# Optimization experiments

Measured on AMD Instinct MI355X. Metric: run time of the kernel, lower is better.

## Reference

```python
import jax, jax.numpy as jnp
import numpy as np

N, C, H, T, D, K = 4096, 512, 128, 64, 20, 10


def setup_inputs() -> dict:
    key = jax.random.key(0)
    ks = jax.random.split(key, 40)
    s = 0.05
    inp = {}
    inp["x"] = jax.random.normal(ks[0], (N, D * T), jnp.float32)
    inp["concept_matrix"] = (jax.random.uniform(ks[1], (N, C)) < 0.05).astype(jnp.float32)
    inp["market_value"] = jax.random.uniform(ks[2], (N,), jnp.float32) + 0.1
    # GRU params (torch layout: w_ih [3H,in], w_hh [3H,H], biases [3H]); 2 layers
    inp["gru_w_ih0"] = jax.random.normal(ks[3], (3 * H, D), jnp.float32) * s
    inp["gru_w_hh0"] = jax.random.normal(ks[4], (3 * H, H), jnp.float32) * s
    inp["gru_b_ih0"] = jax.random.normal(ks[5], (3 * H,), jnp.float32) * s
    inp["gru_b_hh0"] = jax.random.normal(ks[6], (3 * H,), jnp.float32) * s
    inp["gru_w_ih1"] = jax.random.normal(ks[7], (3 * H, H), jnp.float32) * s
    inp["gru_w_hh1"] = jax.random.normal(ks[8], (3 * H, H), jnp.float32) * s
    inp["gru_b_ih1"] = jax.random.normal(ks[9], (3 * H,), jnp.float32) * s
    inp["gru_b_hh1"] = jax.random.normal(ks[10], (3 * H,), jnp.float32) * s
    names = ["ps", "hs", "ps_fore", "hs_fore", "ps_back", "hs_back", "indi"]
    for i, n in enumerate(names):
        inp["w_" + n] = jax.random.normal(ks[11 + 2 * i], (H, H), jnp.float32) * s
        inp["b_" + n] = jax.random.normal(ks[12 + 2 * i], (H,), jnp.float32) * s
    inp["w_out"] = jax.random.normal(ks[30], (1, H), jnp.float32) * s
    inp["b_out"] = jax.random.normal(ks[31], (1,), jnp.float32) * s
    return inp


def _cos_sim(x, y):
    # x [n,d], y [m,d] -> [n,m]; NaN (0/0) replaced by 0 via safe denominator
    xy = x @ y.T
    nx = jnp.sqrt(jnp.sum(x * x, axis=1))[:, None]
    ny = jnp.sqrt(jnp.sum(y * y, axis=1))[:, None]
    return xy / jnp.maximum(nx @ ny.T, 1e-12)


def _gru_layer(seq, wih, whh, bih, bhh):
    # seq [T, n, in] -> outputs [T, n, H]
    n = seq.shape[1]
    h0 = jnp.zeros((n, whh.shape[1]), seq.dtype)

    def step(h, xt):
        gx = xt @ wih.T + bih
        gh = h @ whh.T + bhh
        gxr, gxz, gxn = jnp.split(gx, 3, axis=1)
        ghr, ghz, ghn = jnp.split(gh, 3, axis=1)
        r = jax.nn.sigmoid(gxr + ghr)
        z = jax.nn.sigmoid(gxz + ghz)
        ncand = jnp.tanh(gxn + r * ghn)
        hnew = (1.0 - z) * ncand + z * h
        return hnew, hnew

    _, out = jax.lax.scan(step, h0, seq)
    return out


def reference(x, concept_matrix, market_value,
              gru_w_ih0, gru_w_hh0, gru_b_ih0, gru_b_hh0,
              gru_w_ih1, gru_w_hh1, gru_b_ih1, gru_b_hh1,
              w_ps, b_ps, w_hs, b_hs, w_ps_fore, b_ps_fore, w_hs_fore, b_hs_fore,
              w_ps_back, b_ps_back, w_hs_back, b_hs_back, w_indi, b_indi,
              w_out, b_out):
    n = x.shape[0]
    # [n, D*T] -> [n, D, T] -> [n, T, D] -> [T, n, D]
    seq = jnp.swapaxes(x.reshape(n, D, -1).transpose(0, 2, 1), 0, 1)
    out0 = _gru_layer(seq, gru_w_ih0, gru_w_hh0, gru_b_ih0, gru_b_hh0)
    out1 = _gru_layer(out0, gru_w_ih1, gru_w_hh1, gru_b_ih1, gru_b_hh1)
    x_hidden = out1[-1]  # [n, H]

    # --- predefined-concept branch ---
    s2c = concept_matrix * market_value[:, None]
    s2c_den = jnp.sum(s2c, axis=0)[None, :] * concept_matrix + 1.0
    s2c = s2c / s2c_den
    hidden = s2c.T @ x_hidden  # [C, H]
    v1 = jnp.sum(hidden, axis=1) != 0  # valid concepts (replaces row filtering)
    s2c2 = jax.nn.softmax(x_hidden @ hidden.T, axis=0)  # [n, C], column-wise
    hidden2 = s2c2.T @ x_hidden  # [C, H]
    c2s = _cos_sim(x_hidden, hidden2)
    c2s = jax.nn.softmax(jnp.where(v1[None, :], c2s, -1e9), axis=1) * v1[None, :]
    p_shared = c2s @ hidden2
    p_shared = p_shared @ w_ps.T + b_ps
    p_back = p_shared @ w_ps_back.T + b_ps_back
    out_ps = jax.nn.leaky_relu(p_shared @ w_ps_fore.T + b_ps_fore)

    # --- hidden-concept branch ---
    h_shared = x_hidden - p_back
    hs2c = _cos_sim(h_shared, h_shared)  # [n, n]
    diag = jnp.diagonal(hs2c)
    hs2c = hs2c * (1.0 - jnp.eye(n, dtype=hs2c.dtype))
    _, idx = jax.lax.top_k(hs2c, K)  # [n, K]
    mask = jnp.zeros_like(hs2c).at[jnp.arange(n)[:, None], idx].set(1.0)
    hs2c = hs2c * mask
    hs2c = hs2c + jnp.diag((jnp.sum(hs2c, axis=0) != 0).astype(hs2c.dtype) * diag)
    hidden_h = (h_shared.T @ hs2c).T  # [n, H]
    v2 = jnp.sum(hidden_h, axis=1) != 0
    hc2s = _cos_sim(h_shared, hidden_h)
    hc2s = jax.nn.softmax(jnp.where(v2[None, :], hc2s, -1e9), axis=1) * v2[None, :]
    h_si = hc2s @ hidden_h
    h_si = h_si @ w_hs.T + b_hs
    h_back = h_si @ w_hs_back.T + b_hs_back
    out_hs = jax.nn.leaky_relu(h_si @ w_hs_fore.T + b_hs_fore)

    # --- individual branch + head ---
    indi = x_hidden - p_back - h_back
    out_indi = jax.nn.leaky_relu(indi @ w_indi.T + b_indi)
    all_info = out_ps + out_hs + out_indi
    return (all_info @ w_out.T + b_out).squeeze()
```

## Files before the change

### kernel.cpp

```cpp
#include <hip/hip_runtime.h>
#include <cstddef>

#define NR 4096
#define CDIM 512
#define HDIM 128
#define TSTEPS 64
#define DDIM 20
#define KTOP 10

typedef __attribute__((ext_vector_type(8))) short short8;
typedef __attribute__((ext_vector_type(4))) float f32x4;

__device__ __forceinline__ unsigned short f2bf(float f) {
    union { float f; unsigned u; } x; x.f = f;
    unsigned r = (x.u + 0x7fffu + ((x.u >> 16) & 1u)) >> 16;
    return (unsigned short)r;
}
__device__ __forceinline__ unsigned short f2bf_t(float f) {
    union { float f; unsigned u; } x; x.f = f;
    return (unsigned short)(x.u >> 16);
}
__device__ __forceinline__ float bf2f(unsigned short h) {
    union { unsigned u; float f; } x; x.u = ((unsigned)h) << 16;
    return x.f;
// ... 158 lines not shown
        #pragma unroll
        for (int j = 0; j < 8; j++) {
            float f = src[(size_t)(kb + j) * HDIM + n];
            unsigned short h = f2bf(f);
            knh[(size_t)idx * 8 + j] = h;
            knl[(size_t)idx * 8 + j] = f2bf_t(f - bf2f(h));
        }
    }
}

struct PAll {
    const float* wb_src[4];
    unsigned short* wb_dst[4];
    const float* w7_src[7];
    unsigned short* w7_hi[7];
    unsigned short* w7_lo[7];
};
__global__ void pack_all(PAll p)
{
    int idx = blockIdx.x * 256 + threadIdx.x;
    const int WB_END = 1536 + 3 * 6144;
    if (idx < WB_END) {
        int m, base, nch, K;
        if (idx < 1536) { m = 0; base = 0; nch = 1; K = DDIM; }
        else {
            int q = (idx - 1536) / 6144;
            m = 1 + q;
            base = 1536 + q * 6144;
            nch = 4; K = HDIM;
        }
        int r = idx - base;
        int lane = r & 63;
        int c = (r >> 6) % nch;
        int t = r / (nch * 64);
        int n = t * 16 + (lane & 15);
        int kb = c * 32 + (lane >> 4) * 8;
        const float* W = p.wb_src[m];
        unsigned short* Wp = p.wb_dst[m];
        #pragma unroll
        for (int j = 0; j < 8; j++) {
            int k = kb + j;
            float f = (k < K) ? W[(size_t)n * K + k] : 0.f;
            Wp[(size_t)r * 8 + j] = f2bf(f);
        }
    } else {
        int q = idx - WB_END;
        if (q >= 7 * 2048) return;
        int m = q >> 11;
        int r = q & 2047;
        int lane = r & 63;
        int c = (r >> 6) & 3;
        int t = r >> 8;
        int n = (t << 4) + (lane & 15);
        int kb = (c << 5) + ((lane >> 4) << 3);
        const float* src = p.w7_src[m];
        unsigned short* hi = p.w7_hi[m];
        unsigned short* lo = p.w7_lo[m];
        #pragma unroll
        for (int j = 0; j < 8; j++) {
            float f = src[(size_t)n * HDIM + kb + j];
            unsigned short h = f2bf(f);
            hi[(size_t)r * 8 + j] = h;
            lo[(size_t)r * 8 + j] = f2bf_t(f - bf2f(h));
        }
    }
}

__global__ __launch_bounds__(256) void scan_topk(const float* __restrict__ S,
        const float* __restrict__ hn, float* __restrict__ diagv,
        float* __restrict__ tvals, int* __restrict__ tidx)
{
    int row = blockIdx.x;
    const float* d = S + (size_t)row * NR;
    int tid = threadIdx.x;
    int wv = tid >> 6, lane = tid & 63;
    float hi_ = hn[row];
    float lv[16];
    #pragma unroll
    for (int i = 0; i < 16; i++) {
        int j = tid + (i << 8);
        float v = d[j] / fmaxf(hi_ * hn[j], 1e-12f);
        if (j == row) { diagv[row] = v; v = 0.f; }
        lv[i] = v;
    }
    __shared__ float sv[4];
    __shared__ int si[4];
    for (int k = 0; k < KTOP; k++) {
        float bv = -INFINITY; int bi = 0x7fffffff;
        #pragma unroll
        for (int i = 0; i < 16; i++) {
            int j = tid + (i << 8);
            if (lv[i] > bv || (lv[i] == bv && j < bi)) { bv = lv[i]; bi = j; }
        }
        #pragma unroll
        for (int m = 1; m < 64; m <<= 1) {
            float ov = __shfl_xor(bv, m); int oi = __shfl_xor(bi, m);
            if (ov > bv || (ov == bv && oi < bi)) { bv = ov; bi = oi; }
        }
        if (lane == 0) { sv[wv] = bv; si[wv] = bi; }
        __syncthreads();
        bv = sv[0]; bi = si[0];
        #pragma unroll
        for (int w = 1; w < 4; w++) {
            float ov = sv[w]; int oi = si[w];
            if (ov > bv || (ov == bv && oi < bi)) { bv = ov; bi = oi; }
        }
        if (tid == 0) { tvals[row * KTOP + k] = bv; tidx[row * KTOP + k] = bi; }
        if ((bi & 255) == tid) lv[bi >> 8] = -INFINITY;
        __syncthreads();
    }
}

__global__ __launch_bounds__(512) void hc2s_flash(
    const float* __restrict__ hsh, const float* __restrict__ hn,
    const float* __restrict__ hhn, const float* __restrict__ v2,
    const unsigned short* __restrict__ Bh, const unsigned short* __restrict__ Bl,
    const unsigned short* __restrict__ Vh, const unsigned short* __restrict__ Vl,
    float* __restrict__ pO, float* __restrict__ pM, float* __restrict__ pL)
{
    __shared__ __attribute__((aligned(16))) unsigned short Ph[8][16 * 72];
    __shared__ __attribute__((aligned(16))) unsigned short Plo[8][16 * 72];

    const int tid = threadIdx.x;
    const int wv = tid >> 6, lane = tid & 63, quad = lane >> 4, lm = lane & 15;
    const int rg2 = wv >> 1;
    const int cc = wv & 1;
    const int bm = (blockIdx.x << 6) + (rg2 << 4);
    const int rgg = (blockIdx.x << 2) + rg2;
    const int pidx = (blockIdx.y << 1) + cc;
    const int jt0 = (blockIdx.y << 4) + (cc << 3);

    short8 ahh[4], ahl[4];
    #pragma unroll
    for (int c = 0; c < 4; c++) {
        const float* ap = hsh + (size_t)(bm + lm) * HDIM + (c << 5) + (quad << 3);
        float4 a0 = *(const float4*)ap;
        float4 a1 = *(const float4*)(ap + 4);
        #pragma unroll
        for (int j = 0; j < 4; j++) {
            float f = (&a0.x)[j];
            unsigned short h = f2bf(f);
            ahh[c][j] = h; ahl[c][j] = f2bf_t(f - bf2f(h));
            f = (&a1.x)[j];
            h = f2bf(f);
            ahh[c][4 + j] = h; ahl[c][4 + j] = f2bf_t(f - bf2f(h));
        }
    }
    float hnr[4];
    #pragma unroll
    for (int rg = 0; rg < 4; rg++) hnr[rg] = hn[bm + (quad << 2) + rg];

    float m_old[4], l_old[4];
    #pragma unroll
    for (int rg = 0; rg < 4; rg++) { m_old[rg] = -INFINITY; l_old[rg] = 0.f; }
    f32x4 o[8];
    #pragma unroll
    for (int vt = 0; vt < 8; vt++) o[vt] = (f32x4){0.f, 0.f, 0.f, 0.f};

    const int pwr = lm * 72;
    for (int it = 0; it < 8; it++) {
        const int jt = jt0 + it;
        f32x4 s[4];
        #pragma unroll
        for (int tg = 0; tg < 4; tg++) {
            s[tg] = (f32x4){0.f, 0.f, 0.f, 0.f};
            #pragma unroll
            for (int c = 0; c < 4; c++) {
                size_t bidx = ((size_t)(((jt << 2) + tg) * 4 + c) * 64 + lane) * 8;
                short8 bh = *(const short8*)(Bh + bidx);
                short8 bl = *(const short8*)(Bl + bidx);
                s[tg] = MFMA16(ahh[c], bh, s[tg]);
                s[tg] = MFMA16(ahh[c], bl, s[tg]);
                s[tg] = MFMA16(ahl[c], bh, s[tg]);
            }
        }
        float sv[4][4];
        #pragma unroll
        for (int tg = 0; tg < 4; tg++) {
            int col = (jt << 6) + (tg << 4) + lm;
            float hc = hhn[col];
            float vm = v2[col];
            #pragma unroll
            for (int rg = 0; rg < 4; rg++) {
                float v = s[tg][rg] * __builtin_amdgcn_rcpf(fmaxf(hnr[rg] * hc, 1e-12f));
                sv[tg][rg] = (vm == 0.f) ? -1e9f : v;
            }
        }
        float m_new[4], alpha[4], tsum[4], pv[4][4];
        #pragma unroll
        for (int rg = 0; rg < 4; rg++) {
            float m = fmaxf(fmaxf(sv[0][rg], sv[1][rg]), fmaxf(sv[2][rg], sv[3][rg]));
            #pragma unroll
            for (int d = 1; d < 16; d <<= 1) m = fmaxf(m, __shfl_xor(m, d));
            m_new[rg] = fmaxf(m_old[rg], m);
            alpha[rg] = __expf(m_old[rg] - m_new[rg]);
        }
        #pragma unroll
        for (int rg = 0; rg < 4; rg++) {
            float p0_ = __expf(sv[0][rg] - m_new[rg]);
            float p1_ = __expf(sv[1][rg] - m_new[rg]);
            float p2_ = __expf(sv[2][rg] - m_new[rg]);
            float p3_ = __expf(sv[3][rg] - m_new[rg]);
            pv[0][rg] = p0_; pv[1][rg] = p1_; pv[2][rg] = p2_; pv[3][rg] = p3_;
            float ss = p0_ + p1_ + p2_ + p3_;
            #pragma unroll
            for (int d = 1; d < 16; d <<= 1) ss += __shfl_xor(ss, d);
            tsum[rg] = ss;
        }
        #pragma unroll
        for (int rg = 0; rg < 4; rg++) {
            l_old[rg] = l_old[rg] * alpha[rg] + tsum[rg];
            m_old[rg] = m_new[rg];
        }
        #pragma unroll
        for (int vt = 0; vt < 8; vt++) {
            #pragma unroll
            for (int rg = 0; rg < 4; rg++) o[vt][rg] *= alpha[rg];
        }
        #pragma unroll
        for (int tg = 0; tg < 4; tg++) {
            #pragma unroll
            for (int rg = 0; rg < 4; rg++) {
                int off = ((quad << 2) + rg) * 72 + (tg << 4) + lm;
                float p = pv[tg][rg];
                unsigned short h = f2bf(p);
                Ph[wv][off] = h;
                Plo[wv][off] = f2bf_t(p - bf2f(h));
            }
        }
        __asm__ volatile("s_waitcnt lgkmcnt(0)" ::: "memory");
        #pragma unroll
        for (int c2 = 0; c2 < 2; c2++) {
            int poff = pwr + (c2 << 5) + (quad << 3);
            short8 pah = *(const short8*)&Ph[wv][poff];
            short8 pal = *(const short8*)&Plo[wv][poff];
            int cg = (jt << 1) + c2;
            #pragma unroll
            for (int vt = 0; vt < 8; vt++) {
                size_t b0 = ((size_t)(vt * 128 + cg) * 64 + lane) * 8;
                short8 vh = *(const short8*)(Vh + b0);
                short8 vl = *(const short8*)(Vl + b0);
                o[vt] = MFMA16(pah, vh, o[vt]);
                o[vt] = MFMA16(pah, vl, o[vt]);
                o[vt] = MFMA16(pal, vh, o[vt]);
            }
        }
    }
    size_t pb = ((size_t)rgg * 8 + pidx) * 16;
    #pragma unroll
    for (int rg = 0; rg < 4; rg++) {
        int r = (quad << 2) + rg;
        #pragma unroll
        for (int vt = 0; vt < 8; vt++)
            pO[(pb + r) * 128 + (vt << 4) + lm] = o[vt][rg];
    }
    if (lm == 0) {
        #pragma unroll
        for (int rg = 0; rg < 4; rg++) {
            int r = (quad << 2) + rg;
            pM[pb + r] = m_old[rg];
            pL[pb + r] = l_old[rg];
        }
    }
}

__global__ __launch_bounds__(256) void hc2s_merge(const float* __restrict__ pO,
        const float* __restrict__ pM, const float* __restrict__ pL,
        float* __restrict__ O)
{
    int rgg = blockIdx.x;
    int tid = threadIdx.x;
    int r = tid >> 4;
    int c0 = (tid & 15) << 3;
    float m[8], e[8];
    float M = -INFINITY;
    #pragma unroll
    for (int i = 0; i < 8; i++) {
        m[i] = pM[((size_t)rgg * 8 + i) * 16 + r];
        M = fmaxf(M, m[i]);
    }
    float L = 0.f;
    #pragma unroll
    for (int i = 0; i < 8; i++) {
        e[i] = __expf(m[i] - M);
        L += pL[((size_t)rgg * 8 + i) * 16 + r] * e[i];
    }
    float invL = __builtin_amdgcn_rcpf(L);
    float a[8];
    #pragma unroll
    for (int k = 0; k < 8; k++) a[k] = 0.f;
    #pragma unroll
    for (int i = 0; i < 8; i++) {
        const float* src = pO + (((size_t)rgg * 8 + i) * 16 + r) * 128 + c0;
        float4 v0 = *(const float4*)src;
        float4 v1 = *(const float4*)(src + 4);
        a[0] += v0.x * e[i]; a[1] += v0.y * e[i]; a[2] += v0.z * e[i]; a[3] += v0.w * e[i];
        a[4] += v1.x * e[i]; a[5] += v1.y * e[i]; a[6] += v1.z * e[i]; a[7] += v1.w * e[i];
    }
    float* dst = O + ((size_t)rgg * 16 + r) * 128 + c0;
    #pragma unroll
    for (int k = 0; k < 8; k++) dst[k] = a[k] * invL;
}

__global__ __launch_bounds__(512, 2) void gru_mfma(
    const float* __restrict__ xg,
    const unsigned short* __restrict__ wih0p,
    const unsigned short* __restrict__ whh0p,
    const unsigned short* __restrict__ wih1p,
    const unsigned short* __restrict__ whh1p,
    const float* __restrict__ bih0, const float* __restrict__ bhh0,
    const float* __restrict__ bih1, const float* __restrict__ bhh1,
    float* __restrict__ xh)
{
    __shared__ __attribute__((aligned(16))) unsigned short h0A[2][2][16 * 136];
    __shared__ __attribute__((aligned(16))) unsigned short h1A[2][2][16 * 136];
    __shared__ __attribute__((aligned(16))) unsigned short xA[2][2][16 * 40];

    const int tid = threadIdx.x;
    const int w2 = tid >> 6;
    const int lane = tid & 63;
    const int quad = lane >> 4;
    const int lm = lane & 15;
    const int n0 = blockIdx.x << 4;
    const int j = (w2 << 4) + lm;

    for (int i = tid; i < 2 * 2 * 16 * 136; i += 512) {
        ((unsigned short*)h0A)[i] = 0;
        ((unsigned short*)h1A)[i] = 0;
    }
    for (int i = tid; i < 2 * 2 * 16 * 40; i += 512) ((unsigned short*)xA)[i] = 0;

    float br0 = bih0[j] + bhh0[j];
    float bz0 = bih0[128 + j] + bhh0[128 + j];
    float bni0 = bih0[256 + j];
    float bnh0 = bhh0[256 + j];
    float br1 = bih1[j] + bhh1[j];
    float bz1 = bih1[128 + j] + bhh1[128 + j];
    float bni1 = bih1[256 + j];
    float bnh1 = bhh1[256 + j];

    short8 W0x[3], W0h[3][4], W1x[3][4], W1h[3][4];
    {
        const int lb = lane * 8;
        W0x[0] = *(const short8*)&wih0p[(size_t)(w2) * 512 + lb];
        W0x[1] = *(const short8*)&wih0p[(size_t)(8 + w2) * 512 + lb];
        W0x[2] = *(const short8*)&wih0p[(size_t)(16 + w2) * 512 + lb];
        #pragma unroll
        for (int c = 0; c < 4; c++) {
            W0h[0][c] = *(const short8*)&whh0p[(size_t)((w2) * 4 + c) * 512 + lb];
            W0h[1][c] = *(const short8*)&whh0p[(size_t)((8 + w2) * 4 + c) * 512 + lb];
            W0h[2][c] = *(const short8*)&whh0p[(size_t)((16 + w2) * 4 + c) * 512 + lb];
            W1x[0][c] = *(const short8*)&wih1p[(size_t)((w2) * 4 + c) * 512 + lb];
            W1x[1][c] = *(const short8*)&wih1p[(size_t)((8 + w2) * 4 + c) * 512 + lb];
            W1x[2][c] = *(const short8*)&wih1p[(size_t)((16 + w2) * 4 + c) * 512 + lb];
            W1h[0][c] = *(const short8*)&whh1p[(size_t)((w2) * 4 + c) * 512 + lb];
            W1h[1][c] = *(const short8*)&whh1p[(size_t)((8 + w2) * 4 + c) * 512 + lb];
            W1h[2][c] = *(const short8*)&whh1p[(size_t)((16 + w2) * 4 + c) * 512 + lb];
        }
    }

    const int aoff = lm * 136 + quad * 8;
    const int xoff = lm * 40 + quad * 8;
    const bool stager = tid < 16 * DDIM;
    const int sn = tid / DDIM, sd = tid % DDIM;
    const float* xrow = xg + (size_t)(n0 + sn) * (DDIM * TSTEPS) + sd * TSTEPS;
    const int soff = sn * 40 + sd;

    float h0reg[4] = {0.f, 0.f, 0.f, 0.f};
    float h1reg[4] = {0.f, 0.f, 0.f, 0.f};

    if (stager) {
        float v0 = xrow[0], v1 = xrow[1];
        unsigned short a = f2bf_t(v0);
        xA[0][0][soff] = a; xA[0][1][soff] = f2bf_t(v0 - bf2f(a));
        unsigned short b = f2bf_t(v1);
        xA[1][0][soff] = b; xA[1][1][soff] = f2bf_t(v1 - bf2f(b));
    }
    __syncthreads();

    {
        f32x4 accr = (f32x4){br0, br0, br0, br0};
        f32x4 accz = (f32x4){bz0, bz0, bz0, bz0};
        f32x4 accni = (f32x4){bni0, bni0, bni0, bni0};
        short8 axh = *(const short8*)&xA[0][0][xoff];
        short8 axl = *(const short8*)&xA[0][1][xoff];
        accr = MFMA16(axh, W0x[0], accr);
        accz = MFMA16(axh, W0x[1], accz);
        accni = MFMA16(axh, W0x[2], accni);
        accr = MFMA16(axl, W0x[0], accr);
        accz = MFMA16(axl, W0x[1], accz);
        accni = MFMA16(axl, W0x[2], accni);
        #pragma unroll
        for (int rg = 0; rg < 4; rg++) {
            float r = sigm(accr[rg]);
            float z = sigm(accz[rg]);
            float nc = tanh_f(accni[rg] + r * bnh0);
            float hnew = nc - z * nc;
            h0reg[rg] = hnew;
            int off = (quad * 4 + rg) * 136 + j;
            unsigned short hh_ = f2bf_t(hnew);
            h0A[0][0][off] = hh_;
            h0A[0][1][off] = f2bf_t(hnew - bf2f(hh_));
        }
    }
    __syncthreads();

#define GRU_IT(B, DO_L0, XT, LAST)                                                \
{                                                                                 \
    float xv = 0.f;                                                               \
    if ((XT) >= 0 && stager) xv = xrow[XT];          \
    f32x4 accr0 = (f32x4){br0, br0, br0, br0};                                    \
    f32x4 accz0 = (f32x4){bz0, bz0, bz0, bz0};                                    \
    f32x4 accni0 = (f32x4){bni0, bni0, bni0, bni0};                               \
    f32x4 accnh0 = (f32x4){bnh0, bnh0, bnh0, bnh0};                               \
    f32x4 accr1 = (f32x4){br1, br1, br1, br1};                                    \
    f32x4 accz1 = (f32x4){bz1, bz1, bz1, bz1};                                    \
    f32x4 accni1 = (f32x4){bni1, bni1, bni1, bni1};                               \
    f32x4 accnh1 = (f32x4){bnh1, bnh1, bnh1, bnh1};                               \
    if (DO_L0) {                                                                  \
        short8 axh = *(const short8*)&xA[(B) ^ 1][0][xoff];                       \
        short8 axl = *(const short8*)&xA[(B) ^ 1][1][xoff];                       \
        accr0 = MFMA16(axh, W0x[0], accr0);                                       \
        accz0 = MFMA16(axh, W0x[1], accz0);                                       \
        accni0 = MFMA16(axh, W0x[2], accni0);                                     \
        accr0 = MFMA16(axl, W0x[0], accr0);                                       \
        accz0 = MFMA16(axl, W0x[1], accz0);                                       \
        accni0 = MFMA16(axl, W0x[2], accni0);                                     \
    }                                                                             \
    _Pragma("unroll")                                                             \
    for (int c = 0; c < 4; c++) {                                                 \
        short8 a0h = *(const short8*)&h0A[B][0][aoff + c * 32];                   \
        short8 a0l = *(const short8*)&h0A[B][1][aoff + c * 32];                   \
        short8 a1h = *(const short8*)&h1A[(B) ^ 1][0][aoff + c * 32];             \
        short8 a1l = *(const short8*)&h1A[(B) ^ 1][1][aoff + c * 32];             \
                \
        if (DO_L0) {                                                              \
            accr0 = MFMA16(a0h, W0h[0][c], accr0);                                \
            accz0 = MFMA16(a0h, W0h[1][c], accz0);                                \
            accnh0 = MFMA16(a0h, W0h[2][c], accnh0);                              \
        }                                                                         \
        accr1 = MFMA16(a0h, W1x[0][c], accr1);                                    \
        accz1 = MFMA16(a0h, W1x[1][c], accz1);                                    \
        accni1 = MFMA16(a0h, W1x[2][c], accni1);                                  \
                                                                    \
        if (DO_L0) {                                                              \
            accr0 = MFMA16(a0l, W0h[0][c], accr0);                                \
            accz0 = MFMA16(a0l, W0h[1][c], accz0);                                \
            accnh0 = MFMA16(a0l, W0h[2][c], accnh0);                              \
        }                                                                         \
        accr1 = MFMA16(a0l, W1x[0][c], accr1);                                    \
        accz1 = MFMA16(a0l, W1x[1][c], accz1);                                    \
        accni1 = MFMA16(a0l, W1x[2][c], accni1);                                  \
                                                                    \
        accr1 = MFMA16(a1h, W1h[0][c], accr1);                                    \
        accz1 = MFMA16(a1h, W1h[1][c], accz1);                                    \
        accnh1 = MFMA16(a1h, W1h[2][c], accnh1);                                  \
                                                                    \
        accr1 = MFMA16(a1l, W1h[0][c], accr1);                                    \
        accz1 = MFMA16(a1l, W1h[1][c], accz1);                                    \
        accnh1 = MFMA16(a1l, W1h[2][c], accnh1);                                  \
    }                                                                             \
    if (DO_L0) {                                                                  \
        _Pragma("unroll")                                                         \
        for (int rg = 0; rg < 4; rg++) {                                          \
            float r = sigm(accr0[rg]);                                            \
            float z = sigm(accz0[rg]);                                            \
            float nc = tanh_f(accni0[rg] + r * accnh0[rg]);                       \
            float hnew = nc + z * (h0reg[rg] - nc);                               \
            h0reg[rg] = hnew;                                                     \
            int off = (quad * 4 + rg) * 136 + j;                                  \
            unsigned short hh_ = f2bf_t(hnew);                                    \
            h0A[(B) ^ 1][0][off] = hh_;                                           \
            h0A[(B) ^ 1][1][off] = f2bf_t(hnew - bf2f(hh_));                      \
        }                                                                         \
    }                                                                             \
    _Pragma("unroll")                                                             \
    for (int rg = 0; rg < 4; rg++) {                                              \
        float r = sigm(accr1[rg]);                                                \
        float z = sigm(accz1[rg]);                                                \
        float nc = tanh_f(accni1[rg] + r * accnh1[rg]);                           \
        float hnew = nc + z * (h1reg[rg] - nc);                                   \
        h1reg[rg] = hnew;                                                         \
        if (LAST) {                                                               \
            xh[(size_t)(n0 + quad * 4 + rg) * HDIM + j] = hnew;                   \
        } else {                                                                  \
            int off = (quad * 4 + rg) * 136 + j;                                  \
            unsigned short hh_ = f2bf_t(hnew);                                    \
            h1A[B][0][off] = hh_;                                                 \
            h1A[B][1][off] = f2bf_t(hnew - bf2f(hh_));                            \
        }                                                                         \
    }                                                                             \
    if ((XT) >= 0 && stager) {                                                    \
        unsigned short hh_ = f2bf_t(xv);                                          \
        xA[B][0][soff] = hh_;                                                     \
        xA[B][1][soff] = f2bf_t(xv - bf2f(hh_));                                  \
    }                                                                             \
    if (!(LAST)) __syncthreads();                                                 \
}

    for (int i = 0; i < 62; i += 2) {
        GRU_IT(0, true, i + 2, false)
        GRU_IT(1, true, i + 3, false)
    }
    GRU_IT(0, true, -1, false)
    GRU_IT(1, false, -1, true)
#undef GRU_IT
}

__global__ __launch_bounds__(256) void den_atomic(const float* __restrict__ cm,
        const float* __restrict__ mv, float* __restrict__ den)
{
    int c = blockIdx.x * 64 + (threadIdx.x & 63);
    int rg = threadIdx.x >> 6;
    int nbase = blockIdx.y * 128;
    float acc = 0.f;
    for (int i = 0; i < 32; i++) {
        int n = nbase + rg + (i << 2);
        acc += cm[(size_t)n * CDIM + c] * mv[n];
    }
    __shared__ float red[4][64];
    red[rg][threadIdx.x & 63] = acc;
    __syncthreads();
    if (rg == 0)
        atomicAdd(&den[c], red[0][threadIdx.x] + red[1][threadIdx.x] +
                           red[2][threadIdx.x] + red[3][threadIdx.x]);
}

__global__ __launch_bounds__(256) void s2ct_trans(const float* __restrict__ cm,
        const float* __restrict__ mv, const float* __restrict__ den,
        float* __restrict__ s2cT)
{
    __shared__ float tile[64][65];
    __shared__ float mvs[64];
    const int tid = threadIdx.x;
    const int n0 = blockIdx.x << 6;
    const int c0 = blockIdx.y << 6;
    const int lc = tid & 63, lr = tid >> 6;
    if (tid < 64) mvs[tid] = mv[n0 + tid];
    #pragma unroll
    for (int i = 0; i < 16; i++) {
        int n = lr + (i << 2);
        tile[n][lc] = cm[(size_t)(n0 + n) * CDIM + c0 + lc];
    }
    __syncthreads();
    #pragma unroll
    for (int i = 0; i < 16; i++) {
        int c = lr + (i << 2);
        float m = tile[lc][c];
        float d = den[c0 + c];
        s2cT[(size_t)(c0 + c) * NR + n0 + lc] = (m * mvs[lc]) / (d * m + 1.f);
    }
}

__global__ void row_norm(const float* __restrict__ a, float* __restrict__ out)
{
    int r = blockIdx.x;
    float acc = 0.f;
    for (int h = threadIdx.x; h < HDIM; h += 64) {
        float v = a[(size_t)r * HDIM + h];
        acc += v * v;
    }
    for (int o = 32; o > 0; o >>= 1) acc += __shfl_down(acc, o);
    if (threadIdx.x == 0) out[r] = sqrtf(acc);
}

__global__ void row_nonzero(const float* __restrict__ a, float* __restrict__ out)
{
    int r = blockIdx.x;
    float acc = 0.f;
    for (int h = threadIdx.x; h < HDIM; h += 64) acc += a[(size_t)r * HDIM + h];
    for (int o = 32; o > 0; o >>= 1) acc += __shfl_down(acc, o);
    if (threadIdx.x == 0) out[r] = (acc != 0.f) ? 1.f : 0.f;
}

__global__ void row_norm_nz(const float* __restrict__ a, float* __restrict__ nrm,
                            float* __restrict__ nz)
{
    int r = blockIdx.x;
    float acc = 0.f, s = 0.f;
    for (int h = threadIdx.x; h < HDIM; h += 64) {
        float v = a[(size_t)r * HDIM + h];
        acc += v * v;
        s += v;
    }
    for (int o = 32; o > 0; o >>= 1) { acc += __shfl_down(acc, o); s += __shfl_down(s, o); }
    if (threadIdx.x == 0) { nrm[r] = sqrtf(acc); nz[r] = (s != 0.f) ? 1.f : 0.f; }
}

__global__ __launch_bounds__(256) void cos_softmax_row(float* __restrict__ data, int N,
        const float* __restrict__ rn, const float* __restrict__ cn,
        const float* __restrict__ vmask)
{
    int row = blockIdx.x;
    float* d = data + (size_t)row * N;
    int tid = threadIdx.x;
    int wv = tid >> 6, lane = tid & 63;
    __shared__ float red[8];
    float rnv = rn ? rn[row] : 0.f;
    float mx = -INFINITY;
    for (int j = tid; j < N; j += 256) {
        float v = d[j];
        if (cn) v = v * __builtin_amdgcn_rcpf(fmaxf(rnv * cn[j], 1e-12f));
        if (vmask && vmask[j] == 0.f) v = -1e9f;
        d[j] = v;
        mx = fmaxf(mx, v);
    }
    #pragma unroll
    for (int m = 1; m < 64; m <<= 1) mx = fmaxf(mx, __shfl_xor(mx, m));
    if (lane == 0) red[wv] = mx;
    __syncthreads();
    float M = fmaxf(fmaxf(red[0], red[1]), fmaxf(red[2], red[3]));
    float sum = 0.f;
    for (int j = tid; j < N; j += 256) {
        float e = __expf(d[j] - M);
        d[j] = e;
        sum += e;
    }
    #pragma unroll
    for (int m = 1; m < 64; m <<= 1) sum += __shfl_xor(sum, m);
    if (lane == 0) red[4 + wv] = sum;
    __syncthreads();
    float inv = __builtin_amdgcn_rcpf(red[4] + red[5] + red[6] + red[7]);
    for (int j = tid; j < N; j += 256) {
        float v = d[j] * inv;
        if (vmask) v *= vmask[j];
        d[j] = v;
    }
}

__global__ void hh_scatter(const float* __restrict__ vals, const int* __restrict__ idxs,
                           const float* __restrict__ hsh, float* __restrict__ hh,
                           float* __restrict__ colsum)
{
    int i = blockIdx.x;
    int t = threadIdx.x;
    float hv = hsh[(size_t)i * HDIM + t];
    #pragma unroll
    for (int k = 0; k < KTOP; k++) {
        int p = i * KTOP + k;
        int jj = idxs[p];
        float v = vals[p];
        atomicAdd(&hh[(size_t)jj * HDIM + t], v * hv);
    }
    if (t < KTOP) {
        int p = i * KTOP + t;
        atomicAdd(&colsum[idxs[p]], vals[p]);
    }
}

__global__ void hh_diag(const float* __restrict__ colsum, const float* __restrict__ diag,
                        const float* __restrict__ hsh, float* __restrict__ hh)
{
    int idx = blockIdx.x * 256 + threadIdx.x;
    int j = idx >> 7;
    if (colsum[j] != 0.f) hh[idx] += diag[j] * hsh[idx];
}

static inline void mg(hipStream_t s, const float* A, const unsigned short* Bh,
                      const unsigned short* Bl, const float* bias, float* C,
                      int M, int N, int K, int z, int flags,
                      const float* aux = nullptr, float* sub = nullptr,
                      const unsigned short* Ah = nullptr, const unsigned short* Al = nullptr,
                      const float* wout = nullptr, const float* bout = nullptr,
                      float* hout = nullptr)
{
    MG g{A, Bh, Bl, bias, C, aux, sub, Ah, Al,
         nullptr, nullptr, nullptr, nullptr, wout, bout, hout,
         N, K, K / z, flags | (z > 1 ? 4 : 0) | (Ah ? 16 : 0), 0};
    mfma_gemm<<<dim3(N / 64, M / 64, z), 256, 0, s>>>(g);
}
static inline void mg_dual(hipStream_t s, const float* A,
                           const unsigned short* Bh, const unsigned short* Bl,
                           const float* bias, float* C, int flags1,
                           const unsigned short* Bh2, const unsigned short* Bl2,
                           const float* bias2, float* C2, int flags2,
                           int M, int N, int K,
                           const float* aux, float* sub,
                           const float* wout, const float* bout, float* hout)
{
    MG g{A, Bh, Bl, bias, C, aux, sub, nullptr, nullptr,
         Bh2, Bl2, bias2, C2, wout, bout, hout,
         N, K, K, flags1 | 32, flags2};
    mfma_gemm<<<dim3(N / 64, M / 64, 2), 256, 0, s>>>(g);
}
static inline void pbt(hipStream_t s, const float* src, unsigned short* hi,
                       unsigned short* lo, int N, int K)
{
    int total = (N / 16) * (K / 32) * 64;
    pack_bt<<<(total + 255) / 256, 256, 0, s>>>(src, hi, lo, K, total);
}
static inline void pboth(hipStream_t s, const float* src,
                         unsigned short* bth, unsigned short* btl,
                         unsigned short* knh, unsigned short* knl, int N)
{
    int totBT = (N / 16) * 4 * 64;
    int totKN = 8 * (N / 32) * 64;
    int tot = totBT > totKN ? totBT : totKN;
    pack_both<<<(tot + 255) / 256, 256, 0, s>>>(src, bth, btl, knh, knl, N, totKN);
}

extern "C" void kernel_launch(void* const* d_in, const int* in_sizes, int n_in,
                              void* d_out, int out_size, void* d_ws, size_t ws_size,
                              hipStream_t stream)
{
    (void)in_sizes; (void)n_in; (void)out_size; (void)ws_size;
    const float* x    = (const float*)d_in[0];
    const float* cm   = (const float*)d_in[1];
    const float* mv   = (const float*)d_in[2];
    const float* wih0 = (const float*)d_in[3];
    const float* whh0 = (const float*)d_in[4];
    const float* bih0 = (const float*)d_in[5];
    const float* bhh0 = (const float*)d_in[6];
    const float* wih1 = (const float*)d_in[7];
    const float* whh1 = (const float*)d_in[8];
    const float* bih1 = (const float*)d_in[9];
    const float* bhh1 = (const float*)d_in[10];
    const float* w_ps = (const float*)d_in[11];
    const float* b_ps = (const float*)d_in[12];
    const float* w_hs = (const float*)d_in[13];
    const float* b_hs = (const float*)d_in[14];
    const float* w_ps_fore = (const float*)d_in[15];
    const float* b_ps_fore = (const float*)d_in[16];
    const float* w_hs_fore = (const float*)d_in[17];
    const float* b_hs_fore = (const float*)d_in[18];
    const float* w_ps_back = (const float*)d_in[19];
    const float* b_ps_back = (const float*)d_in[20];
    const float* w_hs_back = (const float*)d_in[21];
    const float* b_hs_back = (const float*)d_in[22];
    const float* w_indi = (const float*)d_in[23];
    const float* b_indi = (const float*)d_in[24];
    const float* w_out  = (const float*)d_in[25];
    const float* b_out  = (const float*)d_in[26];
    float* out = (float*)d_out;

    float* ws = (float*)d_ws;
    float* BIG = ws;
    float* zero0 = ws + 16777216;
    float* den      = zero0;
    float* hidden   = den + 512;
    float* hidden2  = hidden + 65536;
    float* colsum   = hidden2 + 65536;
    float* p0       = colsum + 4096;
    float* hidden_h = p0 + 524288;
    float* p_shared = hidden_h + 524288;
    float* h_si     = p_shared + 524288;
    const size_t ZERO_FLOATS = 512 + 65536 + 65536 + 4096 + 4 * 524288;
    float* h1 = h_si + 524288;
    float* v1 = h1 + 524288;
    float* xnorm = v1 + 512;
    float* h2n = xnorm + 4096;
    float* p_back = h2n + 512;
    float* h_shared = p_back + 524288;
    float* hn = h_shared + 524288;
    float* diagv = hn + 4096;
    float* tvals = diagv + 4096;
    int*   tidx = (int*)(tvals + 40960);
    float* v2 = (float*)(tidx + 40960);
    float* hhn = v2 + 4096;
    float* hsi0 = hhn + 4096;
    float* h_back = hsi0 + 524288;
    float* indi = h_back + 524288;
    float* extra = indi + 524288;

    unsigned short* wih0p = (unsigned short*)(BIG + 5242880);
    unsigned short* whh0p = wih0p + 12288;
    unsigned short* wih1p = whh0p + 49152;
    unsigned short* whh1p = wih1p + 49152;
    float* s2cT = BIG;
    float* L    = BIG + 2097152;
    float* c2s  = BIG + 4194304;
    unsigned short* PB = (unsigned short*)(BIG + 6291456);
    unsigned short* pbt_xh_hi = PB;
    unsigned short* pbt_xh_lo = pbt_xh_hi + 524288;
    unsigned short* pkn_xh_hi = pbt_xh_lo + 524288;
    unsigned short* pkn_xh_lo = pkn_xh_hi + 524288;
    unsigned short* pbt_h2_hi = pkn_xh_lo + 524288;
    unsigned short* pbt_h2_lo = pbt_h2_hi + 65536;
    unsigned short* pkn_h2_hi = pbt_h2_lo + 65536;
    unsigned short* pkn_h2_lo = pkn_h2_hi + 65536;
    unsigned short* wps_hi  = pkn_h2_lo + 65536;
    unsigned short* wps_lo  = wps_hi + 16384;
    unsigned short* wpsb_hi = wps_lo + 16384;
    unsigned short* wpsb_lo = wpsb_hi + 16384;
    unsigned short* wpsf_hi = wpsb_lo + 16384;
    unsigned short* wpsf_lo = wpsf_hi + 16384;
    unsigned short* pbt_hsh_hi = (unsigned short*)p0;
    unsigned short* pbt_hsh_lo = pbt_hsh_hi + 524288;
    unsigned short* pbt_hh_hi = (unsigned short*)indi;
    unsigned short* pbt_hh_lo = pbt_hh_hi + 524288;
    unsigned short* pkn_hh_hi = (unsigned short*)hsi0;
    unsigned short* pkn_hh_lo = pkn_hh_hi + 524288;
    float* part_O = BIG;
    float* part_m = BIG + 4194304;
    float* part_l = BIG + 4227072;
    unsigned short* EX = (unsigned short*)extra;
    unsigned short* whs_hi  = EX;            unsigned short* whs_lo  = EX + 16384;
    unsigned short* whsb_hi = EX + 32768;    unsigned short* whsb_lo = EX + 49152;
    unsigned short* whsf_hi = EX + 65536;    unsigned short* whsf_lo = EX + 81920;
    unsigned short* wind_hi = EX + 98304;    unsigned short* wind_lo = EX + 114688;

    hipMemsetAsync(zero0, 0, ZERO_FLOATS * sizeof(float), stream);
    hipMemsetAsync(out, 0, NR * sizeof(float), stream);

    {
        PAll pa;
        pa.wb_src[0] = wih0; pa.wb_dst[0] = wih0p;
        pa.wb_src[1] = whh0; pa.wb_dst[1] = whh0p;
        pa.wb_src[2] = wih1; pa.wb_dst[2] = wih1p;
        pa.wb_src[3] = whh1; pa.wb_dst[3] = whh1p;
        pa.w7_src[0] = w_ps;      pa.w7_hi[0] = wps_hi;  pa.w7_lo[0] = wps_lo;
        pa.w7_src[1] = w_ps_back; pa.w7_hi[1] = wpsb_hi; pa.w7_lo[1] = wpsb_lo;
        pa.w7_src[2] = w_ps_fore; pa.w7_hi[2] = wpsf_hi; pa.w7_lo[2] = wpsf_lo;
        pa.w7_src[3] = w_hs;      pa.w7_hi[3] = whs_hi;  pa.w7_lo[3] = whs_lo;
        pa.w7_src[4] = w_hs_back; pa.w7_hi[4] = whsb_hi; pa.w7_lo[4] = whsb_lo;
        pa.w7_src[5] = w_hs_fore; pa.w7_hi[5] = whsf_hi; pa.w7_lo[5] = whsf_lo;
        pa.w7_src[6] = w_indi;    pa.w7_hi[6] = wind_hi; pa.w7_lo[6] = wind_lo;
        pack_all<<<134, 256, 0, stream>>>(pa);
    }
    gru_mfma<<<NR / 16, 512, 0, stream>>>(x, wih0p, whh0p, wih1p, whh1p,
                                          bih0, bhh0, bih1, bhh1, h1);
    float* x_hidden = h1;

    den_atomic<<<dim3(CDIM / 64, 32), 256, 0, stream>>>(cm, mv, den);
    s2ct_trans<<<dim3(NR / 64, CDIM / 64), 256, 0, stream>>>(cm, mv, den, s2cT);
    pboth(stream, x_hidden, pbt_xh_hi, pbt_xh_lo, pkn_xh_hi, pkn_xh_lo, NR);
    mg(stream, s2cT, pkn_xh_hi, pkn_xh_lo, nullptr, hidden, CDIM, HDIM, NR, 16, 0);
    row_nonzero<<<CDIM, 64, 0, stream>>>(hidden, v1);
    mg(stream, hidden, pbt_xh_hi, pbt_xh_lo, nullptr, L, CDIM, NR, HDIM, 1, 0);
    cos_softmax_row<<<CDIM, 256, 0, stream>>>(L, NR, nullptr, nullptr, nullptr);
    mg(stream, L, pkn_xh_hi, pkn_xh_lo, nullptr, hidden2, CDIM, HDIM, NR, 16, 0);
    row_norm<<<NR, 64, 0, stream>>>(x_hidden, xnorm);
    row_norm<<<CDIM, 64, 0, stream>>>(hidden2, h2n);
    pboth(stream, hidden2, pbt_h2_hi, pbt_h2_lo, pkn_h2_hi, pkn_h2_lo, CDIM);
    mg(stream, x_hidden, pbt_h2_hi, pbt_h2_lo, nullptr, c2s, NR, CDIM, HDIM, 1, 0,
       nullptr, nullptr, pbt_xh_hi, pbt_xh_lo);
    cos_softmax_row<<<NR, 256, 0, stream>>>(c2s, CDIM, xnorm, h2n, v1);
    mg(stream, c2s, pkn_h2_hi, pkn_h2_lo, nullptr, p0, NR, HDIM, CDIM, 4, 0);
    mg(stream, p0, wps_hi, wps_lo, b_ps, p_shared, NR, HDIM, HDIM, 2, 1);
    mg_dual(stream, p_shared,
            wpsb_hi, wpsb_lo, b_ps_back, p_back, 1 | 8,
            wpsf_hi, wpsf_lo, b_ps_fore, nullptr, 1 | 2 | 64 | 128,
            NR, HDIM, HDIM, x_hidden, h_shared, w_out, b_out, out);

    row_norm<<<NR, 64, 0, stream>>>(h_shared, hn);
    pbt(stream, h_shared, pbt_hsh_hi, pbt_hsh_lo, NR, HDIM);
    mg(stream, h_shared, pbt_hsh_hi, pbt_hsh_lo, nullptr, BIG, NR, NR, HDIM, 1, 0,
       nullptr, nullptr, pbt_hsh_hi, pbt_hsh_lo);
    scan_topk<<<NR, 256, 0, stream>>>(BIG, hn, diagv, tvals, tidx);
    hh_scatter<<<NR, HDIM, 0, stream>>>(tvals, tidx, h_shared, hidden_h, colsum);
    hh_diag<<<2048, 256, 0, stream>>>(colsum, diagv, h_shared, hidden_h);
    row_norm_nz<<<NR, 64, 0, stream>>>(hidden_h, hhn, v2);
    pboth(stream, hidden_h, pbt_hh_hi, pbt_hh_lo, pkn_hh_hi, pkn_hh_lo, NR);
    hc2s_flash<<<dim3(NR / 64, 4), 512, 0, stream>>>(h_shared, hn, hhn, v2,
                                                     pbt_hh_hi, pbt_hh_lo,
                                                     pkn_hh_hi, pkn_hh_lo,
                                                     part_O, part_m, part_l);
    hc2s_merge<<<NR / 16, 256, 0, stream>>>(part_O, part_m, part_l, hsi0);
    mg(stream, hsi0, whs_hi, whs_lo, b_hs, h_si, NR, HDIM, HDIM, 2, 1);
    mg_dual(stream, h_si,
            whsb_hi, whsb_lo, b_hs_back, h_back, 1 | 8,
            whsf_hi, whsf_lo, b_hs_fore, nullptr, 1 | 2 | 64 | 128,
            NR, HDIM, HDIM, h_shared, indi, w_out, b_out, out);

    mg(stream, indi, wind_hi, wind_lo, b_indi, nullptr, NR, HDIM, HDIM, 1,
       1 | 2 | 64 | 128 | 256, nullptr, nullptr, nullptr, nullptr,
       w_out, b_out, out);
}
```

Measured before the change: 671.4 us.

## Split GRU kernel into layer-specialized wavefront groups with 1024-thread blocks

```diff
diff --git a/kernel.cpp b/kernel.cpp
--- a/kernel.cpp
+++ b/kernel.cpp
@@ -484,7 +484,7 @@
     for (int k = 0; k < 8; k++) dst[k] = a[k] * invL;
 }
 
-__global__ __launch_bounds__(512, 2) void gru_mfma(
+__global__ __launch_bounds__(1024) void gru_mfma(
     const float* __restrict__ xg,
     const unsigned short* __restrict__ wih0p,
     const unsigned short* __restrict__ whh0p,
@@ -499,47 +499,27 @@
     __shared__ __attribute__((aligned(16))) unsigned short xA[2][2][16 * 40];
 
     const int tid = threadIdx.x;
-    const int w2 = tid >> 6;
+    const int w4 = tid >> 6;
     const int lane = tid & 63;
     const int quad = lane >> 4;
     const int lm = lane & 15;
     const int n0 = blockIdx.x << 4;
-    const int j = (w2 << 4) + lm;
-
-    for (int i = tid; i < 2 * 2 * 16 * 136; i += 512) {
+    const bool isL0 = (w4 < 8);
+    const int jw = w4 & 7;
+    const int j = (jw << 4) + lm;
+
+    for (int i = tid; i < 2 * 2 * 16 * 136; i += 1024) {
         ((unsigned short*)h0A)[i] = 0;
         ((unsigned short*)h1A)[i] = 0;
     }
-    for (int i = tid; i < 2 * 2 * 16 * 40; i += 512) ((unsigned short*)xA)[i] = 0;
-
-    float br0 = bih0[j] + bhh0[j];
-    float bz0 = bih0[128 + j] + bhh0[128 + j];
-    float bni0 = bih0[256 + j];
-    float bnh0 = bhh0[256 + j];
-    float br1 = bih1[j] + bhh1[j];
-    float bz1 = bih1[128 + j] + bhh1[128 + j];
-    float bni1 = bih1[256 + j];
-    float bnh1 = bhh1[256 + j];
-
-    short8 W0x[3], W0h[3][4], W1x[3][4], W1h[3][4];
-    {
-        const int lb = lane * 8;
-        W0x[0] = *(const short8*)&wih0p[(size_t)(w2) * 512 + lb];
-        W0x[1] = *(const short8*)&wih0p[(size_t)(8 + w2) * 512 + lb];
-        W0x[2] = *(const short8*)&wih0p[(size_t)(16 + w2) * 512 + lb];
-        #pragma unroll
-        for (int c = 0; c < 4; c++) {
-            W0h[0][c] = *(const short8*)&whh0p[(size_t)((w2) * 4 + c) * 512 + lb];
-            W0h[1][c] = *(const short8*)&whh0p[(size_t)((8 + w2) * 4 + c) * 512 + lb];
-            W0h[2][c] = *(const short8*)&whh0p[(size_t)((16 + w2) * 4 + c) * 512 + lb];
-            W1x[0][c] = *(const short8*)&wih1p[(size_t)((w2) * 4 + c) * 512 + lb];
-            W1x[1][c] = *(const short8*)&wih1p[(size_t)((8 + w2) * 4 + c) * 512 + lb];
-            W1x[2][c] = *(const short8*)&wih1p[(size_t)((16 + w2) * 4 + c) * 512 + lb];
-            W1h[0][c] = *(const short8*)&whh1p[(size_t)((w2) * 4 + c) * 512 + lb];
-            W1h[1][c] = *(const short8*)&whh1p[(size_t)((8 + w2) * 4 + c) * 512 + lb];
-            W1h[2][c] = *(const short8*)&whh1p[(size_t)((16 + w2) * 4 + c) * 512 + lb];
-        }
-    }
+    for (int i = tid; i < 2 * 2 * 16 * 40; i += 1024) ((unsigned short*)xA)[i] = 0;
+
+    const float* bihp = isL0 ? bih0 : bih1;
+    const float* bhhp = isL0 ? bhh0 : bhh1;
+    const float br = bihp[j] + bhhp[j];
+    const float bz = bihp[128 + j] + bhhp[128 + j];
+    const float bni = bihp[256 + j];
+    const float bnh = bhhp[256 + j];
 
     const int aoff = lm * 136 + quad * 8;
     const int xoff = lm * 40 + quad * 8;
@@ -547,9 +527,9 @@
     const int sn = tid / DDIM, sd = tid % DDIM;
     const float* xrow = xg + (size_t)(n0 + sn) * (DDIM * TSTEPS) + sd * TSTEPS;
     const int soff = sn * 40 + sd;
-
-    float h0reg[4] = {0.f, 0.f, 0.f, 0.f};
-    float h1reg[4] = {0.f, 0.f, 0.f, 0.f};
+    const int lb = lane * 8;
+
+    float hreg[4] = {0.f, 0.f, 0.f, 0.f};
 
     if (stager) {
         float v0 = xrow[0], v1 = xrow[1];
@@ -560,133 +540,163 @@
     }
     __syncthreads();
 
-    {
-        f32x4 accr = (f32x4){br0, br0, br0, br0};
-        f32x4 accz = (f32x4){bz0, bz0, bz0, bz0};
-        f32x4 accni = (f32x4){bni0, bni0, bni0, bni0};
-        short8 axh = *(const short8*)&xA[0][0][xoff];
-        short8 axl = *(const short8*)&xA[0][1][xoff];
-        accr = MFMA16(axh, W0x[0], accr);
-        accz = MFMA16(axh, W0x[1], accz);
-        accni = MFMA16(axh, W0x[2], accni);
-        accr = MFMA16(axl, W0x[0], accr);
-        accz = MFMA16(axl, W0x[1], accz);
-        accni = MFMA16(axl, W0x[2], accni);
-        #pragma unroll
-        for (int rg = 0; rg < 4; rg++) {
-            float r = sigm(accr[rg]);
-            float z = sigm(accz[rg]);
-            float nc = tanh_f(accni[rg] + r * bnh0);
-            float hnew = nc - z * nc;
-            h0reg[rg] = hnew;
-            int off = (quad * 4 + rg) * 136 + j;
-            unsigned short hh_ = f2bf_t(hnew);
-            h0A[0][0][off] = hh_;
-            h0A[0][1][off] = f2bf_t(hnew - bf2f(hh_));
-        }
-    }
-    __syncthreads();
-
-#define GRU_IT(B, DO_L0, XT, LAST)                                                \
-{                                                                                 \
-    float xv = 0.f;                                                               \
-    if ((XT) >= 0 && stager) xv = xrow[XT];          \
-    f32x4 accr0 = (f32x4){br0, br0, br0, br0};                                    \
-    f32x4 accz0 = (f32x4){bz0, bz0, bz0, bz0};                                    \
-    f32x4 accni0 = (f32x4){bni0, bni0, bni0, bni0};                               \
-    f32x4 accnh0 = (f32x4){bnh0, bnh0, bnh0, bnh0};                               \
-    f32x4 accr1 = (f32x4){br1, br1, br1, br1};                                    \
-    f32x4 accz1 = (f32x4){bz1, bz1, bz1, bz1};                                    \
-    f32x4 accni1 = (f32x4){bni1, bni1, bni1, bni1};                               \
-    f32x4 accnh1 = (f32x4){bnh1, bnh1, bnh1, bnh1};                               \
-    if (DO_L0) {                                                                  \
-        short8 axh = *(const short8*)&xA[(B) ^ 1][0][xoff];                       \
-        short8 axl = *(const short8*)&xA[(B) ^ 1][1][xoff];                       \
-        accr0 = MFMA16(axh, W0x[0], accr0);                                       \
-        accz0 = MFMA16(axh, W0x[1], accz0);                                       \
-        accni0 = MFMA16(axh, W0x[2], accni0);                                     \
-        accr0 = MFMA16(axl, W0x[0], accr0);                                       \
-        accz0 = MFMA16(axl, W0x[1], accz0);                                       \
-        accni0 = MFMA16(axl, W0x[2], accni0);                                     \
-    }                                                                             \
-    _Pragma("unroll")                                                             \
-    for (int c = 0; c < 4; c++) {                                                 \
-        short8 a0h = *(const short8*)&h0A[B][0][aoff + c * 32];                   \
-        short8 a0l = *(const short8*)&h0A[B][1][aoff + c * 32];                   \
-        short8 a1h = *(const short8*)&h1A[(B) ^ 1][0][aoff + c * 32];             \
-        short8 a1l = *(const short8*)&h1A[(B) ^ 1][1][aoff + c * 32];             \
-                \
-        if (DO_L0) {                                                              \
-            accr0 = MFMA16(a0h, W0h[0][c], accr0);                                \
-            accz0 = MFMA16(a0h, W0h[1][c], accz0);                                \
-            accnh0 = MFMA16(a0h, W0h[2][c], accnh0);                              \
-        }                                                                         \
-        accr1 = MFMA16(a0h, W1x[0][c], accr1);                                    \
-        accz1 = MFMA16(a0h, W1x[1][c], accz1);                                    \
-        accni1 = MFMA16(a0h, W1x[2][c], accni1);                                  \
-                                                                    \
-        if (DO_L0) {                                                              \
-            accr0 = MFMA16(a0l, W0h[0][c], accr0);                                \
-            accz0 = MFMA16(a0l, W0h[1][c], accz0);                                \
-            accnh0 = MFMA16(a0l, W0h[2][c], accnh0);                              \
-        }                                                                         \
-        accr1 = MFMA16(a0l, W1x[0][c], accr1);                                    \
-        accz1 = MFMA16(a0l, W1x[1][c], accz1);                                    \
-        accni1 = MFMA16(a0l, W1x[2][c], accni1);                                  \
-                                                                    \
-        accr1 = MFMA16(a1h, W1h[0][c], accr1);                                    \
-        accz1 = MFMA16(a1h, W1h[1][c], accz1);                                    \
-        accnh1 = MFMA16(a1h, W1h[2][c], accnh1);                                  \
-                                                                    \
-        accr1 = MFMA16(a1l, W1h[0][c], accr1);                                    \
-        accz1 = MFMA16(a1l, W1h[1][c], accz1);                                    \
-        accnh1 = MFMA16(a1l, W1h[2][c], accnh1);                                  \
-    }                                                                             \
-    if (DO_L0) {                                                                  \
-        _Pragma("unroll")                                                         \
-        for (int rg = 0; rg < 4; rg++) {                                          \
-            float r = sigm(accr0[rg]);                                            \
-            float z = sigm(accz0[rg]);                                            \
-            float nc = tanh_f(accni0[rg] + r * accnh0[rg]);                       \
-            float hnew = nc + z * (h0reg[rg] - nc);                               \
-            h0reg[rg] = hnew;                                                     \
-            int off = (quad * 4 + rg) * 136 + j;                                  \
-            unsigned short hh_ = f2bf_t(hnew);                                    \
-            h0A[(B) ^ 1][0][off] = hh_;                                           \
-            h0A[(B) ^ 1][1][off] = f2bf_t(hnew - bf2f(hh_));                      \
-        }                                                                         \
-    }                                                                             \
-    _Pragma("unroll")                                                             \
-    for (int rg = 0; rg < 4; rg++) {                                              \
-        float r = sigm(accr1[rg]);                                                \
-        float z = sigm(accz1[rg]);                                                \
-        float nc = tanh_f(accni1[rg] + r * accnh1[rg]);                           \
-        float hnew = nc + z * (h1reg[rg] - nc);                                   \
-        h1reg[rg] = hnew;                                                         \
-        if (LAST) {                                                               \
-            xh[(size_t)(n0 + quad * 4 + rg) * HDIM + j] = hnew;                   \
-        } else {                                                                  \
-            int off = (quad * 4 + rg) * 136 + j;                                  \
-            unsigned short hh_ = f2bf_t(hnew);                                    \
-            h1A[B][0][off] = hh_;                                                 \
-            h1A[B][1][off] = f2bf_t(hnew - bf2f(hh_));                            \
-        }                                                                         \
-    }                                                                             \
-    if ((XT) >= 0 && stager) {                                                    \
-        unsigned short hh_ = f2bf_t(xv);                                          \
-        xA[B][0][soff] = hh_;                                                     \
-        xA[B][1][soff] = f2bf_t(xv - bf2f(hh_));                                  \
-    }                                                                             \
-    if (!(LAST)) __syncthreads();                                                 \
-}
-
-    for (int i = 0; i < 62; i += 2) {
-        GRU_IT(0, true, i + 2, false)
-        GRU_IT(1, true, i + 3, false)
-    }
-    GRU_IT(0, true, -1, false)
-    GRU_IT(1, false, -1, true)
-#undef GRU_IT
+    if (isL0) {
+        short8 Wx0, Wx1, Wx2;
+        short8 Wh[3][4];
+        Wx0 = *(const short8*)&wih0p[(size_t)(jw) * 512 + lb];
+        Wx1 = *(const short8*)&wih0p[(size_t)(8 + jw) * 512 + lb];
+        Wx2 = *(const short8*)&wih0p[(size_t)(16 + jw) * 512 + lb];
+        #pragma unroll
+        for (int g = 0; g < 3; g++) {
+            #pragma unroll
+            for (int c = 0; c < 4; c++)
+                Wh[g][c] = *(const short8*)&whh0p[(size_t)((g * 8 + jw) * 4 + c) * 512 + lb];
+        }
+
+        {
+            f32x4 accr = (f32x4){br, br, br, br};
+            f32x4 accz = (f32x4){bz, bz, bz, bz};
+            f32x4 accni = (f32x4){bni, bni, bni, bni};
+            short8 axh = *(const short8*)&xA[0][0][xoff];
+            short8 axl = *(const short8*)&xA[0][1][xoff];
+            accr = MFMA16(axh, Wx0, accr);
+            accz = MFMA16(axh, Wx1, accz);
+            accni = MFMA16(axh, Wx2, accni);
+            accr = MFMA16(axl, Wx0, accr);
+            accz = MFMA16(axl, Wx1, accz);
+            accni = MFMA16(axl, Wx2, accni);
+            #pragma unroll
+            for (int rg = 0; rg < 4; rg++) {
+                float r = sigm(accr[rg]);
+                float z = sigm(accz[rg]);
+                float nc = tanh_f(accni[rg] + r * bnh);
+                float hnew = nc - z * nc;
+                hreg[rg] = hnew;
+                int off = (quad * 4 + rg) * 136 + j;
+                unsigned short hh_ = f2bf_t(hnew);
+                h0A[0][0][off] = hh_;
+                h0A[0][1][off] = f2bf_t(hnew - bf2f(hh_));
+            }
+        }
+        __syncthreads();
+
+#define L0_IT(B, XT)                                                          \
+{                                                                             \
+    float xv = 0.f;                                                           \
+    if ((XT) >= 0 && stager) xv = xrow[XT];      \
+    f32x4 accr = (f32x4){br, br, br, br};                                     \
+    f32x4 accz = (f32x4){bz, bz, bz, bz};                                     \
+    f32x4 accni = (f32x4){bni, bni, bni, bni};                                \
+    f32x4 accnh = (f32x4){bnh, bnh, bnh, bnh};                                \
+    {                                                                         \
+        short8 axh = *(const short8*)&xA[(B) ^ 1][0][xoff];                   \
+        short8 axl = *(const short8*)&xA[(B) ^ 1][1][xoff];                   \
+        accr = MFMA16(axh, Wx0, accr);                                        \
+        accz = MFMA16(axh, Wx1, accz);                                        \
+        accni = MFMA16(axh, Wx2, accni);                                      \
+        accr = MFMA16(axl, Wx0, accr);                                        \
+        accz = MFMA16(axl, Wx1, accz);                                        \
+        accni = MFMA16(axl, Wx2, accni);                                      \
+    }                                                                         \
+    _Pragma("unroll")                                                         \
+    for (int c = 0; c < 4; c++) {                                             \
+        short8 a0h = *(const short8*)&h0A[B][0][aoff + c * 32];               \
+        short8 a0l = *(const short8*)&h0A[B][1][aoff + c * 32];               \
+        accr = MFMA16(a0h, Wh[0][c], accr);                                   \
+        accz = MFMA16(a0h, Wh[1][c], accz);                                   \
+        accnh = MFMA16(a0h, Wh[2][c], accnh);                                 \
+        accr = MFMA16(a0l, Wh[0][c], accr);                                   \
+        accz = MFMA16(a0l, Wh[1][c], accz);                                   \
+        accnh = MFMA16(a0l, Wh[2][c], accnh);                                 \
+    }                                                                         \
+    _Pragma("unroll")                                                         \
+    for (int rg = 0; rg < 4; rg++) {                                          \
+        float r = sigm(accr[rg]);                                             \
+        float z = sigm(accz[rg]);                                             \
+        float nc = tanh_f(accni[rg] + r * accnh[rg]);                         \
+        float hnew = nc + z * (hreg[rg] - nc);                                \
+        hreg[rg] = hnew;                                                      \
+        int off = (quad * 4 + rg) * 136 + j;                                  \
+        unsigned short hh_ = f2bf_t(hnew);                                    \
+        h0A[(B) ^ 1][0][off] = hh_;                                           \
+        h0A[(B) ^ 1][1][off] = f2bf_t(hnew - bf2f(hh_));                      \
+    }                                                                         \
+    if ((XT) >= 0 && stager) {                                                \
+        unsigned short hh_ = f2bf_t(xv);                                      \
+        xA[B][0][soff] = hh_;                                                 \
+        xA[B][1][soff] = f2bf_t(xv - bf2f(hh_));                              \
+    }                                                                         \
+    __syncthreads();                                                          \
+}
+        for (int i = 0; i < 62; i += 2) {
+            L0_IT(0, i + 2)
+            L0_IT(1, i + 3)
+        }
+        L0_IT(0, -1)
+#undef L0_IT
+    } else {
+        short8 Wx[3][4], Wh[3][4];
+        #pragma unroll
+        for (int g = 0; g < 3; g++) {
+            #pragma unroll
+            for (int c = 0; c < 4; c++) {
+                Wx[g][c] = *(const short8*)&wih1p[(size_t)((g * 8 + jw) * 4 + c) * 512 + lb];
+                Wh[g][c] = *(const short8*)&whh1p[(size_t)((g * 8 + jw) * 4 + c) * 512 + lb];
+            }
+        }
+        __syncthreads();
+
+#define L1_IT(B, LAST)                                                        \
+{                                                                             \
+    f32x4 accr = (f32x4){br, br, br, br};                                     \
+    f32x4 accz = (f32x4){bz, bz, bz, bz};                                     \
+    f32x4 accni = (f32x4){bni, bni, bni, bni};                                \
+    f32x4 accnh = (f32x4){bnh, bnh, bnh, bnh};                                \
+    _Pragma("unroll")                                                         \
+    for (int c = 0; c < 4; c++) {                                             \
+        short8 a0h = *(const short8*)&h0A[B][0][aoff + c * 32];               \
+        short8 a0l = *(const short8*)&h0A[B][1][aoff + c * 32];               \
+        short8 a1h = *(const short8*)&h1A[(B) ^ 1][0][aoff + c * 32];         \
+        short8 a1l = *(const short8*)&h1A[(B) ^ 1][1][aoff + c * 32];         \
+        accr = MFMA16(a0h, Wx[0][c], accr);                                   \
+        accz = MFMA16(a0h, Wx[1][c], accz);                                   \
+        accni = MFMA16(a0h, Wx[2][c], accni);                                 \
+        accr = MFMA16(a0l, Wx[0][c], accr);                                   \
+        accz = MFMA16(a0l, Wx[1][c], accz);                                   \
+        accni = MFMA16(a0l, Wx[2][c], accni);                                 \
+        accr = MFMA16(a1h, Wh[0][c], accr);                                   \
+        accz = MFMA16(a1h, Wh[1][c], accz);                                   \
+        accnh = MFMA16(a1h, Wh[2][c], accnh);                                 \
+        accr = MFMA16(a1l, Wh[0][c], accr);                                   \
+        accz = MFMA16(a1l, Wh[1][c], accz);                                   \
+        accnh = MFMA16(a1l, Wh[2][c], accnh);                                 \
+    }                                                                         \
+    _Pragma("unroll")                                                         \
+    for (int rg = 0; rg < 4; rg++) {                                          \
+        float r = sigm(accr[rg]);                                             \
+        float z = sigm(accz[rg]);                                             \
+        float nc = tanh_f(accni[rg] + r * accnh[rg]);                         \
+        float hnew = nc + z * (hreg[rg] - nc);                                \
+        hreg[rg] = hnew;                                                      \
+        if (LAST) {                                                           \
+            xh[(size_t)(n0 + quad * 4 + rg) * HDIM + j] = hnew;               \
+        } else {                                                              \
+            int off = (quad * 4 + rg) * 136 + j;                              \
+            unsigned short hh_ = f2bf_t(hnew);                                \
+            h1A[B][0][off] = hh_;                                             \
+            h1A[B][1][off] = f2bf_t(hnew - bf2f(hh_));                        \
+        }                                                                     \
+    }                                                                         \
+    if (!(LAST)) __syncthreads();                                             \
+}
+        for (int i = 0; i < 62; i += 2) {
+            L1_IT(0, false)
+            L1_IT(1, false)
+        }
+        L1_IT(0, false)
+        L1_IT(1, true)
+#undef L1_IT
+    }
 }
 
 __global__ __launch_bounds__(256) void den_atomic(const float* __restrict__ cm,
@@ -863,7 +873,7 @@
     MG g{A, Bh, Bl, bias, C, aux, sub, nullptr, nullptr,
          Bh2, Bl2, bias2, C2, wout, bout, hout,
          N, K, K, flags1 | 32, flags2};
-    mfma_gemm<<<dim3(N / 64, M / 64, 2), 256, 0, s>>>(g);
+    mfma_gemm<<<dim3(M / 64 * 0 + N / 64, M / 64, 2), 256, 0, s>>>(g);
 }
 static inline void pbt(hipStream_t s, const float* src, unsigned short* hi,
                        unsigned short* lo, int N, int K)
@@ -999,8 +1009,8 @@
         pa.w7_src[6] = w_indi;    pa.w7_hi[6] = wind_hi; pa.w7_lo[6] = wind_lo;
         pack_all<<<134, 256, 0, stream>>>(pa);
     }
-    gru_mfma<<<NR / 16, 512, 0, stream>>>(x, wih0p, whh0p, wih1p, whh1p,
-                                          bih0, bhh0, bih1, bhh1, h1);
+    gru_mfma<<<NR / 16, 1024, 0, stream>>>(x, wih0p, whh0p, wih1p, whh1p,
+                                           bih0, bhh0, bih1, bhh1, h1);
     float* x_hidden = h1;
 
     den_atomic<<<dim3(CDIM / 64, 32), 256, 0, stream>>>(cm, mv, den);
```

Result: slower. 731.8 us (+9.0%).
